# Performance work log

Measured on AMD Instinct MI355X. Metric: run time of the kernel, lower is better.

## Reference

```python
import jax, jax.numpy as jnp
import numpy as np

EPS = 1e-5
SLOPE = 0.2
K = 20
BINS = [1, 2, 4, 8, 16, 32]


def knn(x_t, k):
    # x_t: (B, N, C) -> idx (B, N, k) of nearest neighbors (by L2, incl. self)
    xx = jnp.sum(x_t * x_t, axis=-1)  # (B, N)
    pd = 2.0 * jnp.einsum('bnc,bmc->bnm', x_t, x_t) - xx[:, :, None] - xx[:, None, :]
    _, idx = jax.lax.top_k(pd, k)
    return idx


def edge_features(x_t, idx):
    # x_t: (B, N, C), idx: (B, N, k) -> (B, N, k, 2C) = [nbr - ctr, ctr]
    B = x_t.shape[0]
    nbr = x_t[jnp.arange(B)[:, None, None], idx]          # (B, N, k, C) gather
    ctr = jnp.broadcast_to(x_t[:, :, None, :], nbr.shape)
    return jnp.concatenate([nbr - ctr, ctr], axis=-1)


def batchnorm(h, gamma, beta, axes):
    # training-mode BN: normalize with batch statistics over `axes` (channel last)
    m = jnp.mean(h, axis=axes, keepdims=True)
    v = jnp.var(h, axis=axes, keepdims=True)
    return (h - m) * jax.lax.rsqrt(v + EPS) * gamma + beta


def lrelu(h):
    return jnp.where(h >= 0, h, SLOPE * h)


def edgeconv(x_t, W, g, b):
    # 1x1 conv over edge features + BN + LeakyReLU + max over k neighbors
    e = edge_features(x_t, knn(x_t, K))            # (B, N, k, 2C)
    h = jnp.einsum('bnkc,oc->bnko', e, W)          # per-edge GEMM
    h = lrelu(batchnorm(h, g, b, (0, 1, 2)))
    return jnp.max(h, axis=2)                      # (B, N, Cout)


def setup_inputs() -> dict:
    key = jax.random.key(0)
    ks = jax.random.split(key, 8)
    B, N = 4, 2048
    d = {'x': jax.random.normal(ks[0], (B, 3, N), dtype=jnp.float32)}
    # conv weights (out, in); BN gamma=1, beta=0 as in torch init
    d['W1'] = jax.random.normal(ks[1], (64, 6), dtype=jnp.float32) * 0.1
    d['g1'] = jnp.ones((64,), jnp.float32); d['b1'] = jnp.zeros((64,), jnp.float32)
    d['W2'] = jax.random.normal(ks[2], (64, 128), dtype=jnp.float32) * 0.1
    d['g2'] = jnp.ones((64,), jnp.float32); d['b2'] = jnp.zeros((64,), jnp.float32)
    d['W3'] = jax.random.normal(ks[3], (128, 128), dtype=jnp.float32) * 0.1
    d['g3'] = jnp.ones((128,), jnp.float32); d['b3'] = jnp.zeros((128,), jnp.float32)
    d['W4'] = jax.random.normal(ks[4], (256, 256), dtype=jnp.float32) * 0.1
    d['g4'] = jnp.ones((256,), jnp.float32); d['b4'] = jnp.zeros((256,), jnp.float32)
    d['W5'] = jax.random.normal(ks[5], (1024, 512), dtype=jnp.float32) * 0.05
    d['g5'] = jnp.ones((1024,), jnp.float32); d['b5'] = jnp.zeros((1024,), jnp.float32)
    d['Wf'] = jax.random.normal(ks[6], (256, 1024), dtype=jnp.float32) * 0.03
    d['bfeat'] = jax.random.normal(ks[7], (256,), dtype=jnp.float32) * 0.01
    return d


def reference(x, W1, g1, b1, W2, g2, b2, W3, g3, b3, W4, g4, b4, W5, g5, b5, Wf, bfeat):
    B, _, N = x.shape
    x_t = jnp.transpose(x, (0, 2, 1))              # (B, N, 3)
    x1 = edgeconv(x_t, W1, g1, b1)                 # (B, N, 64)
    x2 = edgeconv(x1, W2, g2, b2)                  # (B, N, 64)
    x3 = edgeconv(x2, W3, g3, b3)                  # (B, N, 128)
    x4 = edgeconv(x3, W4, g4, b4)                  # (B, N, 256)
    xc = jnp.concatenate([x1, x2, x3, x4], axis=-1)  # (B, N, 512)
    h = jnp.einsum('bnc,oc->bno', xc, W5)          # (B, N, 1024)
    h = lrelu(batchnorm(h, g5, b5, (0, 1)))
    F = h.shape[-1]
    feats = []
    for nb in BINS:  # horizontal pyramid pooling over contiguous point chunks
        z = h.reshape(B, nb, N // nb, F)
        feats.append(jnp.max(z, axis=2) + jnp.mean(z, axis=2))
    bins = jnp.concatenate(feats, axis=1)          # (B, 63, F)
    out = jnp.einsum('bsf,of->sbo', bins, Wf) + bfeat  # (63, B, 256)
    return out
```

## Files before the change

### kernel.cpp

```cpp
#include <hip/hip_runtime.h>
#include <hip/hip_bf16.h>
#include <cstdint>
#include <cstddef>

#define B_SZ   4
#define N_PTS  2048
#define KNN    20
#define BN_ROWS (B_SZ * N_PTS)
#define EPSV   1e-5f
#define SLOPEV 0.2f

#define MODE_GD   0
#define MODE_DIST 1

typedef __attribute__((ext_vector_type(8))) short bf16x8;
typedef __attribute__((ext_vector_type(4))) float f32x4;

__global__ void k_transpose(const float* __restrict__ x, float* __restrict__ xt,
                            float* __restrict__ xx)
{
    int i = blockIdx.x * 256 + threadIdx.x;
    if (i >= BN_ROWS) return;
    int b = i >> 11, n = i & 2047;
    float v0 = x[((b * 3 + 0) << 11) + n];
    float v1 = x[((b * 3 + 1) << 11) + n];
    float v2 = x[((b * 3 + 2) << 11) + n];
    xt[i * 3 + 0] = v0; xt[i * 3 + 1] = v1; xt[i * 3 + 2] = v2;
    xx[i] = fmaf(v0, v0, fmaf(v1, v1, v2 * v2));
}

__global__ void k_prepw_all(const float* __restrict__ W1, const float* __restrict__ W2,
                            const float* __restrict__ W3, const float* __restrict__ W4,
                            const float* __restrict__ W5, const float* __restrict__ Wf,
                            float* __restrict__ wc, __hip_bfloat16* __restrict__ w5h,
                            float* __restrict__ wft)
{
    int i = blockIdx.x * 256 + threadIdx.x;
    if (i >= 876928) return;
    if (i >= 614784) {
        int e = i - 614784;
        int o = e >> 10, f = e & 1023;
        wft[f * 256 + o] = Wf[e];
        return;
    }
    if (i >= 90496) {
        int e = i - 90496;
        w5h[e] = __float2bfloat16(W5[e]);
        return;
    }
    const float* W; int O, C, off;
    if      (i < 384)   { W = W1; O = 64;  C = 3;   off = 0; }
    else if (i < 8576)  { W = W2; O = 64;  C = 64;  off = 384; }
    else if (i < 24960) { W = W3; O = 128; C = 64;  off = 8576; }
    else                { W = W4; O = 256; C = 128; off = 24960; }
    int e = i - off, j = e / C, c = e - j * C;
    float v;
    if (j < O) v = W[j * 2 * C + c];
    else { int jo = j - O; v = W[jo * 2 * C + C + c] - W[jo * 2 * C + c]; }
    wc[i] = v;
}

template<int MODE, bool VEC>
__launch_bounds__(256)
__global__ void k_mm128(const float* __restrict__ A, int lda,
                        const float* __restrict__ Bm, int ldb,
                        const float* __restrict__ xx, int b0,
                        float* __restrict__ C1, float* __restrict__ C2,
                        int Nn, int Kd)
{
    constexpr int LDA_ = 132;
    constexpr int LDB_ = (MODE == MODE_DIST) ? 132 : 68;
    constexpr int SMEMF = 32 * LDA_ + 32 * LDB_;
    __shared__ float smem[SMEMF];
    float* As = smem;
    float* Bs = smem + 32 * LDA_;
    float* T  = smem;
    const int tid = threadIdx.x;
    const int tx  = tid & 15;
    const int ty  = tid >> 4;

    int m0, n0;
    if constexpr (MODE == MODE_DIST) {
        int t = blockIdx.x;
        int it, jt;
        if (t < 120) {
            int i = 0;
            for (; i < 15; ++i) { int cnt = 15 - i; if (t < cnt) break; t -= cnt; }
            it = i; jt = i + 1 + t;
        } else {
            it = jt = t - 120;
        }
        m0 = it * 128;
        n0 = jt * 128;
    } else {
        m0 = blockIdx.y * 128;
        n0 = blockIdx.x * 64;
    }

    const float* Ab;
    const float* Bb;
    int ldbe;
    if constexpr (MODE == MODE_DIST) {
        const int b = b0 + blockIdx.z;
        Ab = A + (size_t)b * N_PTS * lda;
        Bb = Ab;
        ldbe = lda;
    } else {
        Ab = A; Bb = Bm; ldbe = ldb;
    }

    constexpr int NJH = (MODE == MODE_DIST) ? 2 : 1;
    float acc[2][NJH][4][4] = {};

    for (int k0 = 0; k0 < Kd; k0 += 32) {
        #pragma unroll
        for (int r = 0; r < 4; ++r) {
            int e = r * 256 + tid, row = e >> 3, kq = e & 7;
            if constexpr (VEC) {
                float4 v = *(const float4*)&Ab[(size_t)(m0 + row) * lda + k0 + kq * 4];
                As[(kq * 4 + 0) * LDA_ + row] = v.x;
                As[(kq * 4 + 1) * LDA_ + row] = v.y;
                As[(kq * 4 + 2) * LDA_ + row] = v.z;
                As[(kq * 4 + 3) * LDA_ + row] = v.w;
            } else {
                #pragma unroll
                for (int j = 0; j < 4; ++j) {
                    int kg = k0 + kq * 4 + j;
                    As[(kq * 4 + j) * LDA_ + row] =
                        (kg < Kd) ? Ab[(size_t)(m0 + row) * lda + kg] : 0.f;
                }
            }
        }
        constexpr int BR = (MODE == MODE_DIST) ? 4 : 2;
        #pragma unroll
        for (int r = 0; r < BR; ++r) {
            int e = r * 256 + tid, row = e >> 3, kq = e & 7;
            if constexpr (VEC) {
                float4 v = *(const float4*)&Bb[(size_t)(n0 + row) * ldbe + k0 + kq * 4];
                Bs[(kq * 4 + 0) * LDB_ + row] = v.x;
                Bs[(kq * 4 + 1) * LDB_ + row] = v.y;
                Bs[(kq * 4 + 2) * LDB_ + row] = v.z;
                Bs[(kq * 4 + 3) * LDB_ + row] = v.w;
            } else {
                #pragma unroll
                for (int j = 0; j < 4; ++j) {
                    int kg = k0 + kq * 4 + j;
                    Bs[(kq * 4 + j) * LDB_ + row] =
                        (kg < Kd) ? Bb[(size_t)(n0 + row) * ldbe + kg] : 0.f;
                }
            }
        }
        __syncthreads();

        int klen = Kd - k0; if (klen > 32) klen = 32;
        #pragma unroll 8
        for (int kk = 0; kk < klen; ++kk) {
            float4 a0 = *(const float4*)&As[kk * LDA_ + ty * 4];
            float4 a1 = *(const float4*)&As[kk * LDA_ + 64 + ty * 4];
            float av[2][4] = {{a0.x,a0.y,a0.z,a0.w},{a1.x,a1.y,a1.z,a1.w}};
            if constexpr (MODE == MODE_DIST) {
                float4 b0q = *(const float4*)&Bs[kk * LDB_ + tx * 4];
                float4 b1q = *(const float4*)&Bs[kk * LDB_ + 64 + tx * 4];
                float bw[2][4] = {{b0q.x,b0q.y,b0q.z,b0q.w},{b1q.x,b1q.y,b1q.z,b1q.w}};
                #pragma unroll
                for (int ih = 0; ih < 2; ++ih)
                    #pragma unroll
                    for (int jh = 0; jh < 2; ++jh)
                        #pragma unroll
                        for (int ii = 0; ii < 4; ++ii)
                            #pragma unroll
                            for (int jj = 0; jj < 4; ++jj)
                                acc[ih][jh][ii][jj] = fmaf(av[ih][ii], bw[jh][jj], acc[ih][jh][ii][jj]);
            } else {
                float4 bq = *(const float4*)&Bs[kk * LDB_ + tx * 4];
                float bw[4] = {bq.x, bq.y, bq.z, bq.w};
                #pragma unroll
                for (int ih = 0; ih < 2; ++ih)
                    #pragma unroll
                    for (int ii = 0; ii < 4; ++ii)
                        #pragma unroll
                        for (int jj = 0; jj < 4; ++jj)
                            acc[ih][0][ii][jj] = fmaf(av[ih][ii], bw[jj], acc[ih][0][ii][jj]);
            }
        }
        __syncthreads();
    }

    if constexpr (MODE == MODE_DIST) {
        const float* xxb = xx + (b0 + blockIdx.z) * N_PTS;
        float xj[2][4];
        #pragma unroll
        for (int jh = 0; jh < 2; ++jh) {
            float4 v = *(const float4*)&xxb[n0 + jh * 64 + tx * 4];
            xj[jh][0] = v.x; xj[jh][1] = v.y; xj[jh][2] = v.z; xj[jh][3] = v.w;
        }
        float xiv[2][4];
        #pragma unroll
        for (int ih = 0; ih < 2; ++ih)
            #pragma unroll
            for (int i = 0; i < 4; ++i)
                xiv[ih][i] = xxb[m0 + ih * 64 + ty * 4 + i];
        const bool diag = (m0 == n0);
        const size_t zoff = (size_t)blockIdx.z * N_PTS;

        #pragma unroll
        for (int ih = 0; ih < 2; ++ih)
            #pragma unroll
            for (int i = 0; i < 4; ++i) {
                int gi = m0 + ih * 64 + ty * 4 + i;
                float xi = xiv[ih][i];
                size_t base = (zoff + gi) * N_PTS;
                #pragma unroll
                for (int jh = 0; jh < 2; ++jh) {
                    int gj = n0 + jh * 64 + tx * 4;
                    float4 v;
                    v.x = 2.f * acc[ih][jh][i][0] - xi - xj[jh][0];
                    v.y = 2.f * acc[ih][jh][i][1] - xi - xj[jh][1];
                    v.z = 2.f * acc[ih][jh][i][2] - xi - xj[jh][2];
                    v.w = 2.f * acc[ih][jh][i][3] - xi - xj[jh][3];
                    if (diag) {
                        if (gi == gj + 0) v.x = 0.f;
                        if (gi == gj + 1) v.y = 0.f;
                        if (gi == gj + 2) v.z = 0.f;
                        if (gi == gj + 3) v.w = 0.f;
                    }
                    *(float4*)&C1[base + gj] = v;
                }
            }

        if (!diag) {
            #pragma unroll
            for (int jh = 0; jh < 2; ++jh) {
                #pragma unroll
                for (int c = 0; c < 4; ++c) {
                    float xjc = xj[jh][c];
                    #pragma unroll
                    for (int ih = 0; ih < 2; ++ih) {
                        float4 tv;
                        tv.x = 2.f * acc[ih][jh][0][c] - xjc - xiv[ih][0];
                        tv.y = 2.f * acc[ih][jh][1][c] - xjc - xiv[ih][1];
                        tv.z = 2.f * acc[ih][jh][2][c] - xjc - xiv[ih][2];
                        tv.w = 2.f * acc[ih][jh][3][c] - xjc - xiv[ih][3];
                        *(float4*)&T[(tx * 4 + c) * LDA_ + ih * 64 + ty * 4] = tv;
                    }
                }
                __syncthreads();
                #pragma unroll
                for (int r = 0; r < 8; ++r) {
                    int e = r * 256 + tid;
                    int jr = e >> 5, c4 = e & 31;
                    float4 tv = *(const float4*)&T[jr * LDA_ + c4 * 4];
                    *(float4*)&C1[(zoff + n0 + jh * 64 + jr) * N_PTS + m0 + c4 * 4] = tv;
                }
                __syncthreads();
            }
        }
    } else {
        const int Oo = Nn >> 1;
        #pragma unroll
        for (int ih = 0; ih < 2; ++ih)
            #pragma unroll
            for (int i = 0; i < 4; ++i) {
                int row = m0 + ih * 64 + ty * 4 + i;
                int colg = n0 + tx * 4;
                float4 v = make_float4(acc[ih][0][i][0], acc[ih][0][i][1],
                                       acc[ih][0][i][2], acc[ih][0][i][3]);
                if (colg < Oo) *(float4*)&C1[(size_t)row * Oo + colg] = v;
                else           *(float4*)&C2[(size_t)row * Oo + colg - Oo] = v;
            }
    }
}

__launch_bounds__(256)
__global__ void k_gemm5(const unsigned short* __restrict__ Ah,
                        const unsigned short* __restrict__ Bh,
                        float* __restrict__ Cf,
                        float* __restrict__ ssum, float* __restrict__ ssumsq)
{
    constexpr int LDA = 72;
    __shared__ unsigned short As[128 * LDA];
    __shared__ unsigned short Bs[128 * LDA];
    const int tid  = threadIdx.x;
    const int lane = tid & 63;
    const int w    = tid >> 6;
    const int wr   = w >> 1, wcl = w & 1;
    const int quad = lane >> 4;
    const int l16  = lane & 15;
    const int m0 = blockIdx.y * 128;
    const int n0 = blockIdx.x * 128;

    f32x4 acc[4][4] = {};

    for (int k0 = 0; k0 < 512; k0 += 64) {
        #pragma unroll
        for (int r = 0; r < 4; ++r) {
            int e = r * 256 + tid, row = e >> 3, kq = e & 7;
            *(uint4*)&As[row * LDA + kq * 8] =
                *(const uint4*)&Ah[(size_t)(m0 + row) * 512 + k0 + kq * 8];
        }
        #pragma unroll
        for (int r = 0; r < 4; ++r) {
            int e = r * 256 + tid, row = e >> 3, kq = e & 7;
            *(uint4*)&Bs[row * LDA + kq * 8] =
                *(const uint4*)&Bh[(size_t)(n0 + row) * 512 + k0 + kq * 8];
        }
        __syncthreads();
        #pragma unroll
        for (int kk = 0; kk < 64; kk += 32) {
            bf16x8 af[4], bfr[4];
            #pragma unroll
            for (int i = 0; i < 4; ++i)
                af[i] = *(const bf16x8*)&As[(wr * 64 + i * 16 + l16) * LDA + kk + quad * 8];
            #pragma unroll
            for (int j = 0; j < 4; ++j)
                bfr[j] = *(const bf16x8*)&Bs[(wcl * 64 + j * 16 + l16) * LDA + kk + quad * 8];
            #pragma unroll
            for (int i = 0; i < 4; ++i)
                #pragma unroll
                for (int j = 0; j < 4; ++j)
                    acc[i][j] = __builtin_amdgcn_mfma_f32_16x16x32_bf16(af[i], bfr[j], acc[i][j], 0, 0, 0);
        }
        __syncthreads();
    }

    #pragma unroll
    for (int i = 0; i < 4; ++i) {
        int rbase = m0 + wr * 64 + i * 16 + quad * 4;
        #pragma unroll
        for (int j = 0; j < 4; ++j) {
            int col = n0 + wcl * 64 + j * 16 + l16;
            #pragma unroll
            for (int r = 0; r < 4; ++r)
                Cf[(size_t)(rbase + r) * 1024 + col] = acc[i][j][r];
        }
    }

    float* sredS = (float*)As;
    float* sredQ = (float*)Bs;
    #pragma unroll
    for (int j = 0; j < 4; ++j) {
        float s = 0.f, q = 0.f;
        #pragma unroll
        for (int i = 0; i < 4; ++i)
            #pragma unroll
            for (int r = 0; r < 4; ++r) {
                float v = acc[i][j][r];
                s += v; q = fmaf(v, v, q);
            }
        int coll = wcl * 64 + j * 16 + l16;
        int slot = wr * 4 + quad;
        sredS[coll * 8 + slot] = s;
        sredQ[coll * 8 + slot] = q;
    }
    __syncthreads();
    if (tid < 128) {
        float s = 0.f, q = 0.f;
        #pragma unroll
        for (int t = 0; t < 8; ++t) { s += sredS[tid * 8 + t]; q += sredQ[tid * 8 + t]; }
        ssum  [blockIdx.y * 1024 + n0 + tid] = s;
        ssumsq[blockIdx.y * 1024 + n0 + tid] = q;
    }
}

__launch_bounds__(256)
__global__ void k_select(const float* __restrict__ D2, int* __restrict__ idx_out)
{
    const int lane = threadIdx.x & 63;
    const int w    = threadIdx.x >> 6;
    const int qloc = blockIdx.x * 4 + w;
    const float* row = D2 + (size_t)qloc * N_PTS;

    unsigned key[32];
    #pragma unroll
    for (int c = 0; c < 8; ++c) {
        float4 v = *(const float4*)&row[c * 256 + lane * 4];
        float vv[4] = {v.x, v.y, v.z, v.w};
        #pragma unroll
        for (int r = 0; r < 4; ++r) {
            unsigned u = __float_as_uint(vv[r]);
            key[c * 4 + r] = ((int)u >= 0) ? (u | 0x80000000u) : ~u;
        }
    }

    unsigned lo = 0u, hi = 0xFFFFFFFFu;
    while (lo < hi) {
        unsigned mid = lo + ((hi - lo) >> 1);
        int cnt = 0;
        #pragma unroll
        for (int e = 0; e < 32; ++e)
            cnt += __popcll(__ballot(key[e] > mid));
        if (cnt < KNN) hi = mid; else lo = mid + 1;
    }
    const unsigned T = lo;

    int* outp = idx_out + (size_t)qloc * KNN;
    const unsigned long long ltmask = (lane == 0) ? 0ull : (~0ull >> (64 - lane));
    int base = 0;
    #pragma unroll
    for (int e = 0; e < 32; ++e) {
        bool p = key[e] > T;
        unsigned long long m = __ballot(p);
        if (p) {
            int pos = base + __popcll(m & ltmask);
            outp[pos] = (e >> 2) * 256 + lane * 4 + (e & 3);
        }
        base += __popcll(m);
    }
    #pragma unroll
    for (int e = 0; e < 32; ++e) {
        bool p = key[e] == T;
        unsigned long long m = __ballot(p);
        if (p) {
            int pos = base + __popcll(m & ltmask);
            if (pos < KNN) outp[pos] = (e >> 2) * 256 + lane * 4 + (e & 3);
        }
        base += __popcll(m);
    }
}

template<int O, int NSEQ>
__launch_bounds__(256)
__global__ void k_gather(const float* __restrict__ gtab, const float* __restrict__ dtab,
                         const int* __restrict__ idx,
                         float* __restrict__ hmax, float* __restrict__ hmin,
                         float* __restrict__ ssum, float* __restrict__ ssumsq)
{
    constexpr int NPB = 256 / O;
    const int grp = threadIdx.x / O;
    const int o   = threadIdx.x & (O - 1);
    float accS = 0.f, accS2 = 0.f;
    const int rowsPerBlock = NPB * NSEQ;
    const int batch = blockIdx.x & 3;
    const int chunk = blockIdx.x >> 2;
    const int bbase = batch << 11;
    for (int s = 0; s < NSEQ; ++s) {
        int row = bbase + chunk * rowsPerBlock + s * NPB + grp;
        const int* ip = idx + (size_t)row * KNN;
        float gmax = -INFINITY, gmin = INFINITY, gs = 0.f, gs2 = 0.f;
        for (int k = 0; k < KNN; ++k) {
            int nb = ip[k];
            float v = gtab[(size_t)(bbase + nb) * O + o];
            gmax = fmaxf(gmax, v);
            gmin = fminf(gmin, v);
            gs  += v;
            gs2  = fmaf(v, v, gs2);
        }
        float d = dtab[(size_t)row * O + o];
        hmax[(size_t)row * O + o] = gmax + d;
        hmin[(size_t)row * O + o] = gmin + d;
        accS  += gs + (float)KNN * d;
        accS2 += gs2 + 2.f * d * gs + (float)KNN * d * d;
    }
    int bank = blockIdx.x & 63;
    atomicAdd(&ssum[bank * O + o], accS);
    atomicAdd(&ssumsq[bank * O + o], accS2);
}

template<int O, bool WRITE_XX>
__launch_bounds__(256)
__global__ void k_normalize(const float* __restrict__ hmax, const float* __restrict__ hmin,
                            const float* __restrict__ ssum, const float* __restrict__ ssumsq,
                            const float* __restrict__ gamma, const float* __restrict__ beta,
                            float invM, float* __restrict__ xcs,
                            __hip_bfloat16* __restrict__ xch, float* __restrict__ xx)
{
    const int tid = threadIdx.x;
    const int o   = tid & (O - 1);
    float s = 0.f, s2 = 0.f;
    #pragma unroll 8
    for (int bk = 0; bk < 64; ++bk) { s += ssum[bk * O + o]; s2 += ssumsq[bk * O + o]; }
    float mean = s * invM;
    float var  = fmaf(-mean, mean, s2 * invM);
    float sc   = gamma[o] * rsqrtf(var + EPSV);
    float sh   = beta[o] - mean * sc;

    constexpr int R = 256 / O;
    const int rloc = tid / O;
    __shared__ float part[4];
    const int ngroups = BN_ROWS / R;
    for (int gidx = blockIdx.x; gidx < ngroups; gidx += gridDim.x) {
        int row = gidx * R + rloc;
        size_t i = (size_t)row * O + o;
        float h = (sc >= 0.f) ? hmax[i] : hmin[i];
        float y = fmaf(h, sc, sh);
        y = (y >= 0.f) ? y : SLOPEV * y;
        xcs[(size_t)row * 512 + o] = y;
        xch[(size_t)row * 512 + o] = __float2bfloat16(y);
        if constexpr (WRITE_XX) {
            float p = y * y;
            #pragma unroll
            for (int sft = 32; sft >= 1; sft >>= 1) p += __shfl_xor(p, sft, 64);
            if constexpr (O == 64) {
                if ((tid & 63) == 0) xx[row] = p;
            } else {
                if ((tid & 63) == 0) part[tid >> 6] = p;
                __syncthreads();
                if constexpr (O == 128) {
                    if (tid < 2) xx[gidx * R + tid] = part[2 * tid] + part[2 * tid + 1];
                } else {
                    if (tid == 0) xx[gidx * R] = (part[0] + part[1]) + (part[2] + part[3]);
                }
                __syncthreads();
            }
        }
    }
}

__global__ void k_seg(const float* __restrict__ h,
                      const float* __restrict__ ssum, const float* __restrict__ ssumsq,
                      const float* __restrict__ gamma, const float* __restrict__ beta,
                      float* __restrict__ smax, float* __restrict__ ssumseg)
{
    int f = blockIdx.y * 256 + threadIdx.x;
    float s = 0.f, s2 = 0.f;
    #pragma unroll 8
    for (int bk = 0; bk < 64; ++bk) { s += ssum[bk * 1024 + f]; s2 += ssumsq[bk * 1024 + f]; }
    const float invM = 1.f / (float)BN_ROWS;
    float mean = s * invM;
    float var  = fmaf(-mean, mean, s2 * invM);
    float sc   = gamma[f] * rsqrtf(var + EPSV);
    float sh   = beta[f] - mean * sc;

    int seg = blockIdx.x;
    float mx = -INFINITY, sm = 0.f;
    int n0 = seg * 64;
    for (int i = 0; i < 64; ++i) {
        float v = fmaf(h[(size_t)(n0 + i) * 1024 + f], sc, sh);
        v = (v >= 0.f) ? v : SLOPEV * v;
        mx = fmaxf(mx, v); sm += v;
    }
    smax[(size_t)seg * 1024 + f]    = mx;
    ssumseg[(size_t)seg * 1024 + f] = sm;
}

__launch_bounds__(256)
__global__ void k_final(const float* __restrict__ smax, const float* __restrict__ ssg,
                        const float* __restrict__ Wft, const float* __restrict__ bfeat,
                        float* __restrict__ out)
{
    __shared__ float row[1024];
    __shared__ float part[1024];
    const int tid = threadIdx.x;
    int sb = blockIdx.x;
    int s = sb >> 2, b = sb & 3;
    int nb = (s == 0) ? 1 : (s < 3) ? 2 : (s < 7) ? 4 : (s < 15) ? 8 : (s < 31) ? 16 : 32;
    int idxL = s - (nb - 1);
    int segc = 32 / nb;
    int seg0 = b * 32 + idxL * segc;
    float inv = 1.f / (float)(64 * segc);
    for (int c = tid; c < 1024; c += 256) {
        float mx = -INFINITY, sm = 0.f;
        for (int t = 0; t < segc; ++t) {
            mx = fmaxf(mx, smax[(size_t)(seg0 + t) * 1024 + c]);
            sm += ssg[(size_t)(seg0 + t) * 1024 + c];
        }
        row[c] = mx + sm * inv;
    }
    __syncthreads();

    const int lane = tid & 63;
    const int w    = tid >> 6;
    const float* rw = row + w * 256;
    const float* wp = Wft + (size_t)(w * 256) * 256 + lane * 4;
    float4 a0 = {0,0,0,0}, a1 = {0,0,0,0}, a2 = {0,0,0,0}, a3 = {0,0,0,0};
    for (int f = 0; f < 256; f += 4) {
        float r0 = rw[f + 0], r1 = rw[f + 1], r2 = rw[f + 2], r3 = rw[f + 3];
        float4 w0 = *(const float4*)&wp[(size_t)(f + 0) * 256];
        float4 w1 = *(const float4*)&wp[(size_t)(f + 1) * 256];
        float4 w2 = *(const float4*)&wp[(size_t)(f + 2) * 256];
        float4 w3 = *(const float4*)&wp[(size_t)(f + 3) * 256];
        a0.x = fmaf(r0, w0.x, a0.x); a0.y = fmaf(r0, w0.y, a0.y);
        a0.z = fmaf(r0, w0.z, a0.z); a0.w = fmaf(r0, w0.w, a0.w);
        a1.x = fmaf(r1, w1.x, a1.x); a1.y = fmaf(r1, w1.y, a1.y);
        a1.z = fmaf(r1, w1.z, a1.z); a1.w = fmaf(r1, w1.w, a1.w);
        a2.x = fmaf(r2, w2.x, a2.x); a2.y = fmaf(r2, w2.y, a2.y);
        a2.z = fmaf(r2, w2.z, a2.z); a2.w = fmaf(r2, w2.w, a2.w);
        a3.x = fmaf(r3, w3.x, a3.x); a3.y = fmaf(r3, w3.y, a3.y);
        a3.z = fmaf(r3, w3.z, a3.z); a3.w = fmaf(r3, w3.w, a3.w);
    }
    float4 a;
    a.x = (a0.x + a1.x) + (a2.x + a3.x);
    a.y = (a0.y + a1.y) + (a2.y + a3.y);
    a.z = (a0.z + a1.z) + (a2.z + a3.z);
    a.w = (a0.w + a1.w) + (a2.w + a3.w);
    *(float4*)&part[w * 256 + lane * 4] = a;
    __syncthreads();
    int o = tid;
    float acc = (part[o] + part[256 + o]) + (part[512 + o] + part[768 + o]);
    out[(size_t)sb * 256 + o] = acc + bfeat[o];
}

extern "C" void kernel_launch(void* const* d_in, const int* in_sizes, int n_in,
                              void* d_out, int out_size, void* d_ws, size_t ws_size,
                              hipStream_t stream)
{
    const float* x  = (const float*)d_in[0];
    const float* W1 = (const float*)d_in[1];
    const float* g1 = (const float*)d_in[2];
    const float* b1 = (const float*)d_in[3];
    const float* W2 = (const float*)d_in[4];
    const float* g2 = (const float*)d_in[5];
    const float* b2 = (const float*)d_in[6];
    const float* W3 = (const float*)d_in[7];
    const float* g3 = (const float*)d_in[8];
    const float* b3 = (const float*)d_in[9];
    const float* W4 = (const float*)d_in[10];
    const float* g4 = (const float*)d_in[11];
    const float* b4 = (const float*)d_in[12];
    const float* W5 = (const float*)d_in[13];
    const float* g5 = (const float*)d_in[14];
    const float* b5 = (const float*)d_in[15];
    const float* Wf = (const float*)d_in[16];
    const float* bfeat = (const float*)d_in[17];
    float* out = (float*)d_out;
    float* ws  = (float*)d_ws;

    float* xt1   = ws + 0;
    int*   idx   = (int*)(ws + 24576);
    float* xx    = ws + 188416;
    float* xc    = ws + 196608;
    float* hmax  = ws + 4390912;
    float* hmin  = ws + 6488064;
    float* stats = ws + 8585216;
    float* smax  = ws + 8650752;
    float* ssg   = ws + 8781824;
    float* wc    = ws + 8912896;
    float* big   = ws + 9003520;
    float* gtab  = big;
    float* dtab  = big + 2097152;
    __hip_bfloat16* xch = (__hip_bfloat16*)(ws + 25780736);
    __hip_bfloat16* w5h = (__hip_bfloat16*)(ws + 27877888);
    float* wft   = ws + 28140032;
    float* l5s   = ws + 28402176;
    float* l5q   = ws + 28467712;

    hipMemsetAsync(stats, 0, 65536 * sizeof(float), stream);
    k_transpose<<<32, 256, 0, stream>>>(x, xt1, xx);
    k_prepw_all<<<3426, 256, 0, stream>>>(W1, W2, W3, W4, W5, Wf, wc, w5h, wft);

    const float invMk = 1.f / (float)(BN_ROWS * KNN);

    {
        float* ss = stats + 0;
        k_mm128<MODE_DIST, false><<<dim3(136, 1, 4), 256, 0, stream>>>(xt1, 3, nullptr, 0, xx, 0, big, nullptr, N_PTS, 3);
        k_select<<<2048, 256, 0, stream>>>(big, idx);
        k_mm128<MODE_GD, false><<<dim3(2, 64, 1), 256, 0, stream>>>(xt1, 3, wc, 3, nullptr, 0, gtab, dtab, 128, 3);
        k_gather<64, 8><<<256, 256, 0, stream>>>(gtab, dtab, idx, hmax, hmin, ss, ss + 4096);
        k_normalize<64, true><<<512, 256, 0, stream>>>(hmax, hmin, ss, ss + 4096, g1, b1, invMk, xc + 0, xch + 0, xx);
    }
    {
        float* ss = stats + 8192;
        k_mm128<MODE_DIST, true><<<dim3(136, 1, 4), 256, 0, stream>>>(xc + 0, 512, nullptr, 0, xx, 0, big, nullptr, N_PTS, 64);
        k_select<<<2048, 256, 0, stream>>>(big, idx);
        k_mm128<MODE_GD, true><<<dim3(2, 64, 1), 256, 0, stream>>>(xc + 0, 512, wc + 384, 64, nullptr, 0, gtab, dtab, 128, 64);
        k_gather<64, 8><<<256, 256, 0, stream>>>(gtab, dtab, idx, hmax, hmin, ss, ss + 4096);
        k_normalize<64, true><<<512, 256, 0, stream>>>(hmax, hmin, ss, ss + 4096, g2, b2, invMk, xc + 64, xch + 64, xx);
    }
    {
        float* ss = stats + 16384;
        k_mm128<MODE_DIST, true><<<dim3(136, 1, 4), 256, 0, stream>>>(xc + 64, 512, nullptr, 0, xx, 0, big, nullptr, N_PTS, 64);
        k_select<<<2048, 256, 0, stream>>>(big, idx);
        k_mm128<MODE_GD, true><<<dim3(4, 64, 1), 256, 0, stream>>>(xc + 64, 512, wc + 8576, 64, nullptr, 0, gtab, dtab, 256, 64);
        k_gather<128, 8><<<512, 256, 0, stream>>>(gtab, dtab, idx, hmax, hmin, ss, ss + 8192);
        k_normalize<128, true><<<512, 256, 0, stream>>>(hmax, hmin, ss, ss + 8192, g3, b3, invMk, xc + 128, xch + 128, xx);
    }
    {
        float* ss = stats + 32768;
        k_mm128<MODE_DIST, true><<<dim3(136, 1, 4), 256, 0, stream>>>(xc + 128, 512, nullptr, 0, xx, 0, big, nullptr, N_PTS, 128);
        k_select<<<2048, 256, 0, stream>>>(big, idx);
        k_mm128<MODE_GD, true><<<dim3(8, 64, 1), 256, 0, stream>>>(xc + 128, 512, wc + 24960, 128, nullptr, 0, gtab, dtab, 512, 128);
        k_gather<256, 8><<<1024, 256, 0, stream>>>(gtab, dtab, idx, hmax, hmin, ss, ss + 16384);
        k_normalize<256, false><<<512, 256, 0, stream>>>(hmax, hmin, ss, ss + 16384, g4, b4, invMk, xc + 256, xch + 256, xx);
    }
    {
        k_gemm5<<<dim3(8, 64), 256, 0, stream>>>((const unsigned short*)xch, (const unsigned short*)w5h, big, l5s, l5q);
        k_seg<<<dim3(128, 4), 256, 0, stream>>>(big, l5s, l5q, g5, b5, smax, ssg);
        k_final<<<252, 256, 0, stream>>>(smax, ssg, wft, bfeat, out);
    }
}
```

Measured before the change: 576.7 us.

## Register-prefetch next K tile in SIMT GEMM and pair diagonal tiles per block

The shared-memory GEMM now loads the next 32-wide K slice of A and B into registers while computing on the current slice, so global load latency overlaps the FMA loop. Separately, the distance kernel gives each block two diagonal tiles, cutting its grid from 136 to 128 blocks per batch so the block count divides more evenly across CUs. The prefetch costs extra registers per thread, which may lower occupancy, and the paired diagonal blocks run twice as long as the rest.

```diff
diff --git a/kernel.cpp b/kernel.cpp
--- a/kernel.cpp
+++ b/kernel.cpp
@@ -71,6 +71,7 @@
     constexpr int LDA_ = 132;
     constexpr int LDB_ = (MODE == MODE_DIST) ? 132 : 68;
     constexpr int SMEMF = 32 * LDA_ + 32 * LDB_;
+    constexpr int BR = (MODE == MODE_DIST) ? 4 : 2;
     __shared__ float smem[SMEMF];
     float* As = smem;
     float* Bs = smem + 32 * LDA_;
@@ -78,24 +79,6 @@
     const int tid = threadIdx.x;
     const int tx  = tid & 15;
     const int ty  = tid >> 4;
-
-    int m0, n0;
-    if constexpr (MODE == MODE_DIST) {
-        int t = blockIdx.x;
-        int it, jt;
-        if (t < 120) {
-            int i = 0;
-            for (; i < 15; ++i) { int cnt = 15 - i; if (t < cnt) break; t -= cnt; }
-            it = i; jt = i + 1 + t;
-        } else {
-            it = jt = t - 120;
-        }
-        m0 = it * 128;
-        n0 = jt * 128;
-    } else {
-        m0 = blockIdx.y * 128;
-        n0 = blockIdx.x * 64;
-    }
 
     const float* Ab;
     const float* Bb;
@@ -109,165 +92,206 @@
         Ab = A; Bb = Bm; ldbe = ldb;
     }
 
-    constexpr int NJH = (MODE == MODE_DIST) ? 2 : 1;
-    float acc[2][NJH][4][4] = {};
-
-    for (int k0 = 0; k0 < Kd; k0 += 32) {
-        #pragma unroll
-        for (int r = 0; r < 4; ++r) {
-            int e = r * 256 + tid, row = e >> 3, kq = e & 7;
-            if constexpr (VEC) {
-                float4 v = *(const float4*)&Ab[(size_t)(m0 + row) * lda + k0 + kq * 4];
-                As[(kq * 4 + 0) * LDA_ + row] = v.x;
-                As[(kq * 4 + 1) * LDA_ + row] = v.y;
-                As[(kq * 4 + 2) * LDA_ + row] = v.z;
-                As[(kq * 4 + 3) * LDA_ + row] = v.w;
+    const int nt = (MODE == MODE_DIST && blockIdx.x >= 120) ? 2 : 1;
+
+    for (int tt = 0; tt < nt; ++tt) {
+        int m0, n0;
+        if constexpr (MODE == MODE_DIST) {
+            int t = blockIdx.x;
+            if (t < 120) {
+                int i = 0;
+                for (; i < 15; ++i) { int cnt = 15 - i; if (t < cnt) break; t -= cnt; }
+                m0 = i * 128;
+                n0 = (i + 1 + t) * 128;
             } else {
-                #pragma unroll
-                for (int j = 0; j < 4; ++j) {
-                    int kg = k0 + kq * 4 + j;
-                    As[(kq * 4 + j) * LDA_ + row] =
-                        (kg < Kd) ? Ab[(size_t)(m0 + row) * lda + kg] : 0.f;
+                int d = (t - 120) * 2 + tt;
+                m0 = n0 = d * 128;
+            }
+        } else {
+            m0 = blockIdx.y * 128;
+            n0 = blockIdx.x * 64;
+        }
+
+        constexpr int NJH = (MODE == MODE_DIST) ? 2 : 1;
+        float acc[2][NJH][4][4] = {};
+        float4 ra[4], rb[BR];
+
+        auto loadA = [&](int k0) {
+            #pragma unroll
+            for (int r = 0; r < 4; ++r) {
+                int e = r * 256 + tid, row = e >> 3, kq = e & 7;
+                if constexpr (VEC) {
+                    ra[r] = *(const float4*)&Ab[(size_t)(m0 + row) * lda + k0 + kq * 4];
+                } else {
+                    const float* src = &Ab[(size_t)(m0 + row) * lda];
+                    int kb = k0 + kq * 4;
+                    float t0 = (kb + 0 < Kd) ? src[kb + 0] : 0.f;
+                    float t1 = (kb + 1 < Kd) ? src[kb + 1] : 0.f;
+                    float t2 = (kb + 2 < Kd) ? src[kb + 2] : 0.f;
+                    float t3 = (kb + 3 < Kd) ? src[kb + 3] : 0.f;
+                    ra[r] = make_float4(t0, t1, t2, t3);
                 }
             }
-        }
-        constexpr int BR = (MODE == MODE_DIST) ? 4 : 2;
-        #pragma unroll
-        for (int r = 0; r < BR; ++r) {
-            int e = r * 256 + tid, row = e >> 3, kq = e & 7;
-            if constexpr (VEC) {
-                float4 v = *(const float4*)&Bb[(size_t)(n0 + row) * ldbe + k0 + kq * 4];
-                Bs[(kq * 4 + 0) * LDB_ + row] = v.x;
-                Bs[(kq * 4 + 1) * LDB_ + row] = v.y;
-                Bs[(kq * 4 + 2) * LDB_ + row] = v.z;
-                Bs[(kq * 4 + 3) * LDB_ + row] = v.w;
-            } else {
-                #pragma unroll
-                for (int j = 0; j < 4; ++j) {
-                    int kg = k0 + kq * 4 + j;
-                    Bs[(kq * 4 + j) * LDB_ + row] =
-                        (kg < Kd) ? Bb[(size_t)(n0 + row) * ldbe + kg] : 0.f;
+        };
+        auto loadB = [&](int k0) {
+            #pragma unroll
+            for (int r = 0; r < BR; ++r) {
+                int e = r * 256 + tid, row = e >> 3, kq = e & 7;
+                if constexpr (VEC) {
+                    rb[r] = *(const float4*)&Bb[(size_t)(n0 + row) * ldbe + k0 + kq * 4];
+                } else {
+                    const float* src = &Bb[(size_t)(n0 + row) * ldbe];
+                    int kb = k0 + kq * 4;
+                    float t0 = (kb + 0 < Kd) ? src[kb + 0] : 0.f;
+                    float t1 = (kb + 1 < Kd) ? src[kb + 1] : 0.f;
+                    float t2 = (kb + 2 < Kd) ? src[kb + 2] : 0.f;
+                    float t3 = (kb + 3 < Kd) ? src[kb + 3] : 0.f;
+                    rb[r] = make_float4(t0, t1, t2, t3);
                 }
             }
-        }
-        __syncthreads();
-
-        int klen = Kd - k0; if (klen > 32) klen = 32;
-        #pragma unroll 8
-        for (int kk = 0; kk < klen; ++kk) {
-            float4 a0 = *(const float4*)&As[kk * LDA_ + ty * 4];
-            float4 a1 = *(const float4*)&As[kk * LDA_ + 64 + ty * 4];
-            float av[2][4] = {{a0.x,a0.y,a0.z,a0.w},{a1.x,a1.y,a1.z,a1.w}};
-            if constexpr (MODE == MODE_DIST) {
-                float4 b0q = *(const float4*)&Bs[kk * LDB_ + tx * 4];
-                float4 b1q = *(const float4*)&Bs[kk * LDB_ + 64 + tx * 4];
-                float bw[2][4] = {{b0q.x,b0q.y,b0q.z,b0q.w},{b1q.x,b1q.y,b1q.z,b1q.w}};
-                #pragma unroll
-                for (int ih = 0; ih < 2; ++ih)
+        };
+        auto writeAB = [&]() {
+            #pragma unroll
+            for (int r = 0; r < 4; ++r) {
+                int e = r * 256 + tid, row = e >> 3, kq = e & 7;
+                As[(kq * 4 + 0) * LDA_ + row] = ra[r].x;
+                As[(kq * 4 + 1) * LDA_ + row] = ra[r].y;
+                As[(kq * 4 + 2) * LDA_ + row] = ra[r].z;
+                As[(kq * 4 + 3) * LDA_ + row] = ra[r].w;
+            }
+            #pragma unroll
+            for (int r = 0; r < BR; ++r) {
+                int e = r * 256 + tid, row = e >> 3, kq = e & 7;
+                Bs[(kq * 4 + 0) * LDB_ + row] = rb[r].x;
+                Bs[(kq * 4 + 1) * LDB_ + row] = rb[r].y;
+                Bs[(kq * 4 + 2) * LDB_ + row] = rb[r].z;
+                Bs[(kq * 4 + 3) * LDB_ + row] = rb[r].w;
+            }
+        };
+
+        loadA(0); loadB(0);
+        for (int k0 = 0; k0 < Kd; k0 += 32) {
+            writeAB();
+            __syncthreads();
+            if (k0 + 32 < Kd) { loadA(k0 + 32); loadB(k0 + 32); }
+
+            int klen = Kd - k0; if (klen > 32) klen = 32;
+            #pragma unroll 8
+            for (int kk = 0; kk < klen; ++kk) {
+                float4 a0 = *(const float4*)&As[kk * LDA_ + ty * 4];
+                float4 a1 = *(const float4*)&As[kk * LDA_ + 64 + ty * 4];
+                float av[2][4] = {{a0.x,a0.y,a0.z,a0.w},{a1.x,a1.y,a1.z,a1.w}};
+                if constexpr (MODE == MODE_DIST) {
+                    float4 b0q = *(const float4*)&Bs[kk * LDB_ + tx * 4];
+                    float4 b1q = *(const float4*)&Bs[kk * LDB_ + 64 + tx * 4];
+                    float bw[2][4] = {{b0q.x,b0q.y,b0q.z,b0q.w},{b1q.x,b1q.y,b1q.z,b1q.w}};
                     #pragma unroll
-                    for (int jh = 0; jh < 2; ++jh)
+                    for (int ih = 0; ih < 2; ++ih)
+                        #pragma unroll
+                        for (int jh = 0; jh < 2; ++jh)
+                            #pragma unroll
+                            for (int ii = 0; ii < 4; ++ii)
+                                #pragma unroll
+                                for (int jj = 0; jj < 4; ++jj)
+                                    acc[ih][jh][ii][jj] = fmaf(av[ih][ii], bw[jh][jj], acc[ih][jh][ii][jj]);
+                } else {
+                    float4 bq = *(const float4*)&Bs[kk * LDB_ + tx * 4];
+                    float bw[4] = {bq.x, bq.y, bq.z, bq.w};
+                    #pragma unroll
+                    for (int ih = 0; ih < 2; ++ih)
                         #pragma unroll
                         for (int ii = 0; ii < 4; ++ii)
                             #pragma unroll
                             for (int jj = 0; jj < 4; ++jj)
-                                acc[ih][jh][ii][jj] = fmaf(av[ih][ii], bw[jh][jj], acc[ih][jh][ii][jj]);
-            } else {
-                float4 bq = *(const float4*)&Bs[kk * LDB_ + tx * 4];
-                float bw[4] = {bq.x, bq.y, bq.z, bq.w};
+                                acc[ih][0][ii][jj] = fmaf(av[ih][ii], bw[jj], acc[ih][0][ii][jj]);
+                }
+            }
+            __syncthreads();
+        }
+
+        if constexpr (MODE == MODE_DIST) {
+            const float* xxb = xx + (b0 + blockIdx.z) * N_PTS;
+            float xj[2][4];
+            #pragma unroll
+            for (int jh = 0; jh < 2; ++jh) {
+                float4 v = *(const float4*)&xxb[n0 + jh * 64 + tx * 4];
+                xj[jh][0] = v.x; xj[jh][1] = v.y; xj[jh][2] = v.z; xj[jh][3] = v.w;
+            }
+            float xiv[2][4];
+            #pragma unroll
+            for (int ih = 0; ih < 2; ++ih)
                 #pragma unroll
-                for (int ih = 0; ih < 2; ++ih)
+                for (int i = 0; i < 4; ++i)
+                    xiv[ih][i] = xxb[m0 + ih * 64 + ty * 4 + i];
+            const bool diag = (m0 == n0);
+            const size_t zoff = (size_t)blockIdx.z * N_PTS;
+
+            #pragma unroll
+            for (int ih = 0; ih < 2; ++ih)
+                #pragma unroll
+                for (int i = 0; i < 4; ++i) {
+                    int gi = m0 + ih * 64 + ty * 4 + i;
+                    float xi = xiv[ih][i];
+                    size_t base = (zoff + gi) * N_PTS;
                     #pragma unroll
-                    for (int ii = 0; ii < 4; ++ii)
-                        #pragma unroll
-                        for (int jj = 0; jj < 4; ++jj)
-                            acc[ih][0][ii][jj] = fmaf(av[ih][ii], bw[jj], acc[ih][0][ii][jj]);
-            }
-        }
-        __syncthreads();
-    }
-
-    if constexpr (MODE == MODE_DIST) {
-        const float* xxb = xx + (b0 + blockIdx.z) * N_PTS;
-        float xj[2][4];
-        #pragma unroll
-        for (int jh = 0; jh < 2; ++jh) {
-            float4 v = *(const float4*)&xxb[n0 + jh * 64 + tx * 4];
-            xj[jh][0] = v.x; xj[jh][1] = v.y; xj[jh][2] = v.z; xj[jh][3] = v.w;
-        }
-        float xiv[2][4];
-        #pragma unroll
-        for (int ih = 0; ih < 2; ++ih)
-            #pragma unroll
-            for (int i = 0; i < 4; ++i)
-                xiv[ih][i] = xxb[m0 + ih * 64 + ty * 4 + i];
-        const bool diag = (m0 == n0);
-        const size_t zoff = (size_t)blockIdx.z * N_PTS;
-
-        #pragma unroll
-        for (int ih = 0; ih < 2; ++ih)
-            #pragma unroll
-            for (int i = 0; i < 4; ++i) {
-                int gi = m0 + ih * 64 + ty * 4 + i;
-                float xi = xiv[ih][i];
-                size_t base = (zoff + gi) * N_PTS;
+                    for (int jh = 0; jh < 2; ++jh) {
+                        int gj = n0 + jh * 64 + tx * 4;
+                        float4 v;
+                        v.x = 2.f * acc[ih][jh][i][0] - xi - xj[jh][0];
+                        v.y = 2.f * acc[ih][jh][i][1] - xi - xj[jh][1];
+                        v.z = 2.f * acc[ih][jh][i][2] - xi - xj[jh][2];
+                        v.w = 2.f * acc[ih][jh][i][3] - xi - xj[jh][3];
+                        if (diag) {
+                            if (gi == gj + 0) v.x = 0.f;
+                            if (gi == gj + 1) v.y = 0.f;
+                            if (gi == gj + 2) v.z = 0.f;
+                            if (gi == gj + 3) v.w = 0.f;
+                        }
+                        *(float4*)&C1[base + gj] = v;
+                    }
+                }
+
+            if (!diag) {
                 #pragma unroll
                 for (int jh = 0; jh < 2; ++jh) {
-                    int gj = n0 + jh * 64 + tx * 4;
-                    float4 v;
-                    v.x = 2.f * acc[ih][jh][i][0] - xi - xj[jh][0];
-                    v.y = 2.f * acc[ih][jh][i][1] - xi - xj[jh][1];
-                    v.z = 2.f * acc[ih][jh][i][2] - xi - xj[jh][2];
-                    v.w = 2.f * acc[ih][jh][i][3] - xi - xj[jh][3];
-                    if (diag) {
-                        if (gi == gj + 0) v.x = 0.f;
-                        if (gi == gj + 1) v.y = 0.f;
-                        if (gi == gj + 2) v.z = 0.f;
-                        if (gi == gj + 3) v.w = 0.f;
+                    #pragma unroll
+                    for (int c = 0; c < 4; ++c) {
+                        float xjc = xj[jh][c];
+                        #pragma unroll
+                        for (int ih = 0; ih < 2; ++ih) {
+                            float4 tv;
+                            tv.x = 2.f * acc[ih][jh][0][c] - xjc - xiv[ih][0];
+                            tv.y = 2.f * acc[ih][jh][1][c] - xjc - xiv[ih][1];
+                            tv.z = 2.f * acc[ih][jh][2][c] - xjc - xiv[ih][2];
+                            tv.w = 2.f * acc[ih][jh][3][c] - xjc - xiv[ih][3];
+                            *(float4*)&T[(tx * 4 + c) * LDA_ + ih * 64 + ty * 4] = tv;
+                        }
                     }
-                    *(float4*)&C1[base + gj] = v;
+                    __syncthreads();
+                    #pragma unroll
+                    for (int r = 0; r < 8; ++r) {
+                        int e = r * 256 + tid;
+                        int jr = e >> 5, c4 = e & 31;
+                        float4 tv = *(const float4*)&T[jr * LDA_ + c4 * 4];
+                        *(float4*)&C1[(zoff + n0 + jh * 64 + jr) * N_PTS + m0 + c4 * 4] = tv;
+                    }
+                    __syncthreads();
                 }
             }
-
-        if (!diag) {
-            #pragma unroll
-            for (int jh = 0; jh < 2; ++jh) {
+        } else {
+            const int Oo = Nn >> 1;
+            #pragma unroll
+            for (int ih = 0; ih < 2; ++ih)
                 #pragma unroll
-                for (int c = 0; c < 4; ++c) {
-                    float xjc = xj[jh][c];
-                    #pragma unroll
-                    for (int ih = 0; ih < 2; ++ih) {
-                        float4 tv;
-                        tv.x = 2.f * acc[ih][jh][0][c] - xjc - xiv[ih][0];
-                        tv.y = 2.f * acc[ih][jh][1][c] - xjc - xiv[ih][1];
-                        tv.z = 2.f * acc[ih][jh][2][c] - xjc - xiv[ih][2];
-                        tv.w = 2.f * acc[ih][jh][3][c] - xjc - xiv[ih][3];
-                        *(float4*)&T[(tx * 4 + c) * LDA_ + ih * 64 + ty * 4] = tv;
-                    }
+                for (int i = 0; i < 4; ++i) {
+                    int row = m0 + ih * 64 + ty * 4 + i;
+                    int colg = n0 + tx * 4;
+                    float4 v = make_float4(acc[ih][0][i][0], acc[ih][0][i][1],
+                                           acc[ih][0][i][2], acc[ih][0][i][3]);
+                    if (colg < Oo) *(float4*)&C1[(size_t)row * Oo + colg] = v;
+                    else           *(float4*)&C2[(size_t)row * Oo + colg - Oo] = v;
                 }
-                __syncthreads();
-                #pragma unroll
-                for (int r = 0; r < 8; ++r) {
-                    int e = r * 256 + tid;
-                    int jr = e >> 5, c4 = e & 31;
-                    float4 tv = *(const float4*)&T[jr * LDA_ + c4 * 4];
-                    *(float4*)&C1[(zoff + n0 + jh * 64 + jr) * N_PTS + m0 + c4 * 4] = tv;
-                }
-                __syncthreads();
-            }
-        }
-    } else {
-        const int Oo = Nn >> 1;
-        #pragma unroll
-        for (int ih = 0; ih < 2; ++ih)
-            #pragma unroll
-            for (int i = 0; i < 4; ++i) {
-                int row = m0 + ih * 64 + ty * 4 + i;
-                int colg = n0 + tx * 4;
-                float4 v = make_float4(acc[ih][0][i][0], acc[ih][0][i][1],
-                                       acc[ih][0][i][2], acc[ih][0][i][3]);
-                if (colg < Oo) *(float4*)&C1[(size_t)row * Oo + colg] = v;
-                else           *(float4*)&C2[(size_t)row * Oo + colg - Oo] = v;
-            }
+        }
     }
 }
 
@@ -642,7 +666,7 @@
 
     {
         float* ss = stats + 0;
-        k_mm128<MODE_DIST, false><<<dim3(136, 1, 4), 256, 0, stream>>>(xt1, 3, nullptr, 0, xx, 0, big, nullptr, N_PTS, 3);
+        k_mm128<MODE_DIST, false><<<dim3(128, 1, 4), 256, 0, stream>>>(xt1, 3, nullptr, 0, xx, 0, big, nullptr, N_PTS, 3);
         k_select<<<2048, 256, 0, stream>>>(big, idx);
         k_mm128<MODE_GD, false><<<dim3(2, 64, 1), 256, 0, stream>>>(xt1, 3, wc, 3, nullptr, 0, gtab, dtab, 128, 3);
         k_gather<64, 8><<<256, 256, 0, stream>>>(gtab, dtab, idx, hmax, hmin, ss, ss + 4096);
@@ -650,7 +674,7 @@
     }
     {
         float* ss = stats + 8192;
-        k_mm128<MODE_DIST, true><<<dim3(136, 1, 4), 256, 0, stream>>>(xc + 0, 512, nullptr, 0, xx, 0, big, nullptr, N_PTS, 64);
+        k_mm128<MODE_DIST, true><<<dim3(128, 1, 4), 256, 0, stream>>>(xc + 0, 512, nullptr, 0, xx, 0, big, nullptr, N_PTS, 64);
         k_select<<<2048, 256, 0, stream>>>(big, idx);
         k_mm128<MODE_GD, true><<<dim3(2, 64, 1), 256, 0, stream>>>(xc + 0, 512, wc + 384, 64, nullptr, 0, gtab, dtab, 128, 64);
         k_gather<64, 8><<<256, 256, 0, stream>>>(gtab, dtab, idx, hmax, hmin, ss, ss + 4096);
@@ -658,7 +682,7 @@
     }
     {
         float* ss = stats + 16384;
-        k_mm128<MODE_DIST, true><<<dim3(136, 1, 4), 256, 0, stream>>>(xc + 64, 512, nullptr, 0, xx, 0, big, nullptr, N_PTS, 64);
+        k_mm128<MODE_DIST, true><<<dim3(128, 1, 4), 256, 0, stream>>>(xc + 64, 512, nullptr, 0, xx, 0, big, nullptr, N_PTS, 64);
         k_select<<<2048, 256, 0, stream>>>(big, idx);
         k_mm128<MODE_GD, true><<<dim3(4, 64, 1), 256, 0, stream>>>(xc + 64, 512, wc + 8576, 64, nullptr, 0, gtab, dtab, 256, 64);
         k_gather<128, 8><<<512, 256, 0, stream>>>(gtab, dtab, idx, hmax, hmin, ss, ss + 8192);
@@ -666,7 +690,7 @@
     }
     {
         float* ss = stats + 32768;
-        k_mm128<MODE_DIST, true><<<dim3(136, 1, 4), 256, 0, stream>>>(xc + 128, 512, nullptr, 0, xx, 0, big, nullptr, N_PTS, 128);
+        k_mm128<MODE_DIST, true><<<dim3(128, 1, 4), 256, 0, stream>>>(xc + 128, 512, nullptr, 0, xx, 0, big, nullptr, N_PTS, 128);
         k_select<<<2048, 256, 0, stream>>>(big, idx);
         k_mm128<MODE_GD, true><<<dim3(8, 64, 1), 256, 0, stream>>>(xc + 128, 512, wc + 24960, 128, nullptr, 0, gtab, dtab, 512, 128);
         k_gather<256, 8><<<1024, 256, 0, stream>>>(gtab, dtab, idx, hmax, hmin, ss, ss + 16384);
```

Measured after the change: 591.2 us. 1.03x slower.
